# Performance work log

Measured on AMD Instinct MI355X. Metric: run time of the kernel, lower is better.

Reference implementation:

```python
import jax, jax.numpy as jnp
import numpy as np

# ---- module configuration (from init_kwargs) ----
NX, NV = 2048, 1024
LX = 1.0
VMAX = 6.0
DX = LX / NX
DV = 2.0 * VMAX / NV
XS = jnp.linspace(-LX / 2 + DX / 2, LX / 2 - DX / 2, NX)
VS = jnp.linspace(-VMAX + DV / 2, VMAX - DV / 2, NV)
AE, AI = 1.0, 1836.0
ZE, ZI = -1.0, 1.0
OMEGA_C_TAU = 1.0
NU_EE, NU_II = 1.0, 0.1
DT = 1e-3
T_LBO = 1.0  # LBO temperature, u = 0


def minmod(a, b):
    return jnp.where(a * b > 0, jnp.sign(a) * jnp.minimum(jnp.abs(a), jnp.abs(b)), 0.0)


def _sl(a, lo, hi, axis):
    return jax.lax.slice_in_dim(a, lo, hi, axis=axis)


def slope_limited_flux_divergence(f_pad, F, dx, axis):
    # f_pad has N+4 cells along `axis` (2 ghost cells per side). MUSCL + minmod.
    n = f_pad.shape[axis]
    d = _sl(f_pad, 1, n, axis) - _sl(f_pad, 0, n - 1, axis)          # n-1 diffs
    sigma = minmod(_sl(d, 0, n - 2, axis), _sl(d, 1, n - 1, axis))    # slopes for cells 1..n-2
    fc = _sl(f_pad, 1, n - 1, axis)                                   # cells 1..n-2
    m = n - 2
    fL = _sl(fc, 0, m - 1, axis) + 0.5 * _sl(sigma, 0, m - 1, axis)   # left interface states
    fR = _sl(fc, 1, m, axis) - 0.5 * _sl(sigma, 1, m, axis)           # right interface states
    flux = F(fL, fR)                                                  # N+1 interface fluxes
    k = flux.shape[axis]
    return (_sl(flux, 1, k, axis) - _sl(flux, 0, k - 1, axis)) / dx   # N cells


def pad_x_periodic(f):
    return jnp.concatenate([f[-2:, :], f, f[:2, :]], axis=0)


def pad_v_zero(f):
    z = jnp.zeros((f.shape[0], 2), f.dtype)
    return jnp.concatenate([z, f, z], axis=1)


def poisson_solve(rho_c):
    # dE/dx = rho_c, zero-mean E (periodic-compatible gauge)
    E = jnp.cumsum(rho_c) * DX
    return E - jnp.mean(E)


def species_rhs(f, E, A, Z):
    v = VS[None, :]
    Fx = lambda l, r: jnp.where(v > 0, l * v, r * v)                  # upwind in x
    vdfdx = slope_limited_flux_divergence(pad_x_periodic(f), Fx, DX, axis=0)
    Ec = (OMEGA_C_TAU * Z / A) * E[:, None]
    Fv = lambda l, r: jnp.where(Ec > 0, l * Ec, r * Ec)               # upwind in v
    Edfdv = slope_limited_flux_divergence(pad_v_zero(f), Fv, DV, axis=1)
    return -vdfdx - Edfdv


def vlasov_rhs(fe, fi):
    ne = jnp.sum(fe, axis=1) * DV
    ni = jnp.sum(fi, axis=1) * DV
    E = poisson_solve(ZE * ne + ZI * ni)
    return species_rhs(fe, E, AE, ZE), species_rhs(fi, E, AI, ZI)


def ssprk2(fe, fi, dt):
    re, ri = vlasov_rhs(fe, fi)
    fe1, fi1 = fe + dt * re, fi + dt * ri
    re1, ri1 = vlasov_rhs(fe1, fi1)
    return 0.5 * (fe + fe1 + dt * re1), 0.5 * (fi + fi1 + dt * ri1)


def lbo_diagonals(lam):
    # L f = lam * d/dv( v f + T df/dv ), central differences
    vm = jnp.roll(VS, 1)
    vp = jnp.roll(VS, -1)
    dl = lam * (T_LBO / DV**2 - vm / (2 * DV))
    du = lam * (T_LBO / DV**2 + vp / (2 * DV))
    d = lam * (-2.0 * T_LBO / DV**2) * jnp.ones(NV, XS.dtype)
    return dl.at[0].set(0.0), d, du.at[-1].set(0.0)


def nu_shape():
    midpt = LX / 3
    ef = LX / 6 / 10
    h0 = lambda x: 1 + jnp.exp(x / ef - midpt / ef)
    return 1.0 / (0.5 * (h0(XS) + h0(-XS)))  # [Nx]


def thomas(dl, d, du, b):
    # Thomas algorithm; dl[0]==0 and du[-1]==0 assumed.
    def fwd(carry, inp):
        cp, bp = carry
        dli, di, dui, bi = inp
        m = di - dli * cp
        cpi = dui / m
        bpi = (bi - dli * bp) / m
        return (cpi, bpi), (cpi, bpi)
    z = jnp.zeros((), b.dtype)
    _, (cp, bp) = jax.lax.scan(fwd, (z, z), (dl, d, du, b))
    def bwd(x_next, inp):
        cpi, bpi = inp
        x = bpi - cpi * x_next
        return x, x
    _, x = jax.lax.scan(bwd, z, (cp, bp), reverse=True)
    return x


def implicit_collide(f, lam, dt):
    dl, d, du = lbo_diagonals(lam)
    nu = nu_shape()
    def solve_row(nui, frow):
        return thomas(-dt * nui * dl, 1.0 - dt * nui * d, -dt * nui * du, frow)
    return jax.vmap(solve_row)(nu, f)


def setup_inputs() -> dict:
    key = jax.random.key(0)
    k1, k2 = jax.random.split(key)
    fe = jax.random.uniform(k1, (NX, NV), dtype=jnp.float32)
    fi = jax.random.uniform(k2, (NX, NV), dtype=jnp.float32)
    return {"fe": fe, "fi": fi}


def reference(fe, fi):
    fe1, fi1 = ssprk2(fe, fi, DT)
    fe2 = implicit_collide(fe1, NU_EE, DT)
    fi2 = implicit_collide(fi1, NU_II, DT)
    return jnp.stack([fe2, fi2])  # [2, Nx, Nv]
```

## Files before the change

kernel.cpp:

```cpp
#include <hip/hip_runtime.h>
#include <math.h>

#define NX 2048
#define NV 1024

static constexpr float DXf    = 1.0f / 2048.0f;
static constexpr float DVf    = 12.0f / 1024.0f;
static constexpr float DTf    = 0.001f;
static constexpr float INV_DX = 2048.0f;
static constexpr float INV_DV = 1024.0f / 12.0f;

__device__ __forceinline__ float minmod_f(float a, float b) {
    return (a * b > 0.0f) ? (a > 0.0f ? fminf(a, b) : fmaxf(a, b)) : 0.0f;
}

__device__ __forceinline__ float frcp(float x) {
    float r = __builtin_amdgcn_rcpf(x);
    return r * (2.0f - x * r);
}

__device__ __forceinline__ int swz512(int x) {
    return ((x & 7) << 6) + (x >> 3);
}

__device__ __forceinline__ void rhs4(const float* __restrict__ g, int i, int j0, float Ec,
                                     float4& f0v, float4& rv) {
    const float* rowc = g + i * NV;
    const float* rm1  = g + (((i - 1) & (NX - 1)) * NV);
    const float* rm2  = g + (((i - 2) & (NX - 1)) * NV);
    const float* rp1  = g + (((i + 1) & (NX - 1)) * NV);
    const float* rp2  = g + (((i + 2) & (NX - 1)) * NV);

    float4 c   = *(const float4*)(rowc + j0);
    float4 xm1 = *(const float4*)(rm1 + j0);
    float4 xm2 = *(const float4*)(rm2 + j0);
    float4 xp1 = *(const float4*)(rp1 + j0);
    float4 xp2 = *(const float4*)(rp2 + j0);
    float4 lm = make_float4(0.f, 0.f, 0.f, 0.f);
    float4 rp = make_float4(0.f, 0.f, 0.f, 0.f);
    if (j0 >= 4)      lm = *(const float4*)(rowc + j0 - 4);
    if (j0 <= NV - 8) rp = *(const float4*)(rowc + j0 + 4);

    float vals[8] = {lm.z, lm.w, c.x, c.y, c.z, c.w, rp.x, rp.y};
    const float* cc   = (const float*)&c;
    const float* am1  = (const float*)&xm1;
    const float* am2  = (const float*)&xm2;
    const float* ap1  = (const float*)&xp1;
    const float* ap2  = (const float*)&xp2;
    float* f0o = (float*)&f0v;
    float* ro  = (float*)&rv;

    #pragma unroll
    for (int k = 0; k < 4; ++k) {
        float f0  = cc[k];
        float fm1 = am1[k], fm2 = am2[k], fp1 = ap1[k], fp2 = ap2[k];

        float v = DVf * ((float)(j0 + k) + 0.5f) - 6.0f;
        float dm1 = fm1 - fm2, d0 = f0 - fm1, dp1 = fp1 - f0, dp2 = fp2 - fp1;
        float sm1 = minmod_f(dm1, d0);
        float s0  = minmod_f(d0, dp1);
        float sp1 = minmod_f(dp1, dp2);
        float PhiM, PhiP;
        if (v > 0.0f) {
            PhiM = (fm1 + 0.5f * sm1) * v;
            PhiP = (f0  + 0.5f * s0 ) * v;
        } else {
            PhiM = (f0  - 0.5f * s0 ) * v;
            PhiP = (fp1 - 0.5f * sp1) * v;
        }
        float vdfdx = (PhiP - PhiM) * INV_DX;

        float gm2 = vals[k], gm1 = vals[k + 1], gp1 = vals[k + 3], gp2 = vals[k + 4];
        float em1 = gm1 - gm2, e0 = f0 - gm1, ep1 = gp1 - f0, ep2 = gp2 - gp1;
        float tm1 = minmod_f(em1, e0);
        float t0  = minmod_f(e0, ep1);
        float tp1 = minmod_f(ep1, ep2);
        float GM, GP;
        if (Ec > 0.0f) {
            GM = (gm1 + 0.5f * tm1) * Ec;
            GP = (f0  + 0.5f * t0 ) * Ec;
        } else {
            GM = (f0  - 0.5f * t0 ) * Ec;
            GP = (gp1 - 0.5f * tp1) * Ec;
        }
        float Edfdv = (GP - GM) * INV_DV;

        f0o[k] = f0;
        ro[k]  = -vdfdx - Edfdv;
    }
}

__device__ __forceinline__ float block_E(const float* __restrict__ se_,
                                         const float* __restrict__ si_,
                                         int r0, int wv) {
    int t = threadIdx.x;
    int i3 = r0 + 3;
    float pref = 0.0f, wtot = 0.0f;
    #pragma unroll
    for (int q = 0; q < NX / 256; ++q) {
        int k = q * 256 + t;
        float rho = DVf * (si_[k] - se_[k]);
        if (k <= i3) pref += rho;
        wtot += rho * (float)(NX - k);
    }
    #pragma unroll
    for (int off = 32; off > 0; off >>= 1) {
        pref += __shfl_down(pref, off, 64);
        wtot += __shfl_down(wtot, off, 64);
    }
    __shared__ float sp_[4], sw_[4];
    int lane = t & 63, wave = t >> 6;
    if (lane == 0) { sp_[wave] = pref; sw_[wave] = wtot; }
    __syncthreads();
    float P3 = sp_[0] + sp_[1] + sp_[2] + sp_[3];
    float W  = sw_[0] + sw_[1] + sw_[2] + sw_[3];
    float rho1 = DVf * (si_[r0 + 1] - se_[r0 + 1]);
    float rho2 = DVf * (si_[r0 + 2] - se_[r0 + 2]);
    float rho3 = DVf * (si_[r0 + 3] - se_[r0 + 3]);
    float corr = (wv == 3) ? 0.0f
               : (wv == 2) ? rho3
               : (wv == 1) ? (rho3 + rho2)
                           : (rho3 + rho2 + rho1);
    return DXf * (P3 - corr - W * (1.0f / (float)NX));
}

__global__ __launch_bounds__(256) void moments_kernel(const float* __restrict__ fe,
                                                      const float* __restrict__ fi,
                                                      float* __restrict__ se,
                                                      float* __restrict__ si) {
    const int g = swz512(blockIdx.x);
    const int t = threadIdx.x, lane = t & 63, wv = t >> 6;
    const int row = (g << 2) + wv;
    const float* rpe = fe + row * NV;
    const float* rpi = fi + row * NV;
    float a = 0.0f, b = 0.0f;
    #pragma unroll
    for (int q = 0; q < 4; ++q) {
        float4 x = *(const float4*)(rpe + 4 * lane + 256 * q);
        float4 y = *(const float4*)(rpi + 4 * lane + 256 * q);
        a += x.x + x.y + x.z + x.w;
        b += y.x + y.y + y.z + y.w;
    }
    #pragma unroll
    for (int off = 32; off > 0; off >>= 1) {
        a += __shfl_down(a, off, 64);
        b += __shfl_down(b, off, 64);
    }
    if (lane == 0) { se[row] = a; si[row] = b; }
}

__global__ __launch_bounds__(256) void stage1_kernel(const float* __restrict__ fe,
                                                     const float* __restrict__ fi,
                                                     const float* __restrict__ se,
                                                     const float* __restrict__ si,
                                                     float* __restrict__ fe1,
                                                     float* __restrict__ fi1,
                                                     float* __restrict__ se1,
                                                     float* __restrict__ si1) {
    const int g  = swz512(blockIdx.x);
    const int sp = blockIdx.y;
    const int r0 = g << 2;
    const int t = threadIdx.x, lane = t & 63, wv = t >> 6;
    const float* f = sp ? fi : fe;
    float* f1 = sp ? fi1 : fe1;
    const float zoa = sp ? (1.0f / 1836.0f) : -1.0f;
    const float Ec = zoa * block_E(se, si, r0, wv);
    const int row = r0 + wv;

    float s = 0.0f;
    #pragma unroll
    for (int q = 0; q < 4; ++q) {
        const int j0 = 4 * lane + 256 * q;
        float4 f0v, rv;
        rhs4(f, row, j0, Ec, f0v, rv);
        float4 o;
        o.x = f0v.x + DTf * rv.x;
        o.y = f0v.y + DTf * rv.y;
        o.z = f0v.z + DTf * rv.z;
        o.w = f0v.w + DTf * rv.w;
        *(float4*)(f1 + row * NV + j0) = o;
        s += o.x + o.y + o.z + o.w;
    }
    #pragma unroll
    for (int off = 32; off > 0; off >>= 1) s += __shfl_down(s, off, 64);
    if (lane == 0) (sp ? si1 : se1)[row] = s;
}

__global__ __launch_bounds__(256) void stage2_collide_kernel(
    const float* __restrict__ fe, const float* __restrict__ fi,
    const float* __restrict__ fe1, const float* __restrict__ fi1,
    const float* __restrict__ se1, const float* __restrict__ si1,
    float* __restrict__ out) {
    const int g  = swz512(blockIdx.x);
    const int sp = blockIdx.y;
    const int r0 = g << 2;
    const int t = threadIdx.x, lane = t & 63, wv = t >> 6;
    const float* h  = sp ? fi : fe;
    const float* f1 = sp ? fi1 : fe1;
    const float zoa = sp ? (1.0f / 1836.0f) : -1.0f;
    const float lam = sp ? 0.1f : 1.0f;
    const float Ec = zoa * block_E(se1, si1, r0, wv);
    const int row = r0 + wv;
    float* orow = out + ((size_t)sp * NX + row) * NV;

    const float Tdv2   = 1.0f / (DVf * DVf);
    const float inv2dv = 0.5f / DVf;
    const float xi = DXf * ((float)row + 0.5f) - 0.5f;
    const float nu = 1.0f / (1.0f + 0.5f * (expf(60.0f * xi - 20.0f) + expf(-60.0f * xi - 20.0f)));
    const float K = DTf * nu * lam;
    const float b = 1.0f + 2.0f * K * Tdv2;

    const int j0 = 16 * lane;

    float Dv[16], Av[16], Cv[16];
    #pragma unroll
    for (int q = 0; q < 4; ++q) {
        float4 f0v, rv;
        rhs4(f1, row, j0 + 4 * q, Ec, f0v, rv);
        float4 h4 = *(const float4*)(h + row * NV + j0 + 4 * q);
        float dq[4];
        dq[0] = 0.5f * h4.x + 0.5f * f0v.x + (0.5f * DTf) * rv.x;
        dq[1] = 0.5f * h4.y + 0.5f * f0v.y + (0.5f * DTf) * rv.y;
        dq[2] = 0.5f * h4.z + 0.5f * f0v.z + (0.5f * DTf) * rv.z;
        dq[3] = 0.5f * h4.w + 0.5f * f0v.w + (0.5f * DTf) * rv.w;
        #pragma unroll
        for (int rr = 0; rr < 4; ++rr) {
            const int r = 4 * q + rr;
            const int j = j0 + r;
            float a = (j == 0)      ? 0.0f : -K * (Tdv2 - (DVf * ((float)j - 0.5f) - 6.0f) * inv2dv);
            float c = (j == NV - 1) ? 0.0f : -K * (Tdv2 + (DVf * ((float)j + 1.5f) - 6.0f) * inv2dv);
            if (r == 0) {
                float e = frcp(b);
                Dv[0] = e * dq[0];
                Av[0] = e * a;
                Cv[0] = e * c;
            } else {
                float e = frcp(b - a * Cv[r - 1]);
                Dv[r] = e * (dq[rr] - a * Dv[r - 1]);
                Av[r] = -e * a * Av[r - 1];
                Cv[r] = e * c;
            }
        }
    }
    #pragma unroll
    for (int r = 14; r >= 0; --r) {
        Dv[r] = Dv[r] - Cv[r] * Dv[r + 1];
        Av[r] = Av[r] - Cv[r] * Av[r + 1];
        Cv[r] = -Cv[r] * Cv[r + 1];
    }

    float la = Av[0],  ra = Cv[0],  d0 = Dv[0];
    float lb = Av[15], rb = Cv[15], d1 = Dv[15];
    #pragma unroll
    for (int s = 1; s < 64; s <<= 1) {
        float lb_m = __shfl_up(lb, s, 64);
        float rb_m = __shfl_up(rb, s, 64);
        float d1_m = __shfl_up(d1, s, 64);
        if (lane < s) { lb_m = 0.0f; rb_m = 0.0f; d1_m = 0.0f; }
        float la_p = __shfl_down(la, s, 64);
        float ra_p = __shfl_down(ra, s, 64);
        float d0_p = __shfl_down(d0, s, 64);
        if (lane + s > 63) { la_p = 0.0f; ra_p = 0.0f; d0_p = 0.0f; }

        float m00 = 1.0f - la * rb_m;
        float m01 = -ra * la_p;
        float m10 = -lb * rb_m;
        float m11 = 1.0f - rb * la_p;
        float idet = frcp(m00 * m11 - m01 * m10);

        float Lr0 = -la * lb_m, Lr1 = -lb * lb_m;
        float Rr0 = -ra * ra_p, Rr1 = -rb * ra_p;
        float e0 = d0 - la * d1_m - ra * d0_p;
        float e1 = d1 - lb * d1_m - rb * d0_p;

        la = idet * (m11 * Lr0 - m01 * Lr1);
        lb = idet * (m00 * Lr1 - m10 * Lr0);
        ra = idet * (m11 * Rr0 - m01 * Rr1);
        rb = idet * (m00 * Rr1 - m10 * Rr0);
        d0 = idet * (m11 * e0 - m01 * e1);
        d1 = idet * (m00 * e1 - m10 * e0);
    }
    float zl = __shfl_up(d1, 1, 64);
    if (lane == 0) zl = 0.0f;
    float yr = __shfl_down(d0, 1, 64);
    if (lane == 63) yr = 0.0f;

    #pragma unroll
    for (int r = 0; r < 16; ++r) Dv[r] = Dv[r] - Av[r] * zl - Cv[r] * yr;
    #pragma unroll
    for (int q = 0; q < 4; ++q) {
        float4 o;
        o.x = Dv[4 * q + 0];
        o.y = Dv[4 * q + 1];
        o.z = Dv[4 * q + 2];
        o.w = Dv[4 * q + 3];
        *(float4*)(orow + j0 + 4 * q) = o;
    }
}

extern "C" void kernel_launch(void* const* d_in, const int* in_sizes, int n_in,
                              void* d_out, int out_size, void* d_ws, size_t ws_size,
                              hipStream_t stream) {
    const float* fe = (const float*)d_in[0];
    const float* fi = (const float*)d_in[1];
    float* out = (float*)d_out;
    const size_t P = (size_t)NX * NV;

    float* fe1 = (float*)d_ws;
    float* fi1 = fe1 + P;
    float* se  = fi1 + P;
    float* si  = se + NX;
    float* se1 = si + NX;
    float* si1 = se1 + NX;

    dim3 rgrid(512, 2);

    moments_kernel<<<512, 256, 0, stream>>>(fe, fi, se, si);
    stage1_kernel<<<rgrid, 256, 0, stream>>>(fe, fi, se, si, fe1, fi1, se1, si1);
    stage2_collide_kernel<<<rgrid, 256, 0, stream>>>(fe, fi, fe1, fi1, se1, si1, out);
}
```

Measured before the change: 127.5 us.

## Precompute E field via single-block scan kernel and use one row per block

Replaces the per-block redundant reduction over all 2048 charge densities (block_E) with a separate single-block prefix-scan kernel that writes E once per stage. The stage kernels then read E[row] directly, and the grid is restructured so each block handles one row (256 threads for moments/stage1, one 64-thread wave for stage2), giving 4x more blocks. This removes redundant per-block work and a barrier, at the cost of two extra serial tiny launches and smaller blocks.

```diff
diff --git a/kernel.cpp b/kernel.cpp
--- a/kernel.cpp
+++ b/kernel.cpp
@@ -19,8 +19,8 @@
     return r * (2.0f - x * r);
 }
 
-__device__ __forceinline__ int swz512(int x) {
-    return ((x & 7) << 6) + (x >> 3);
+__device__ __forceinline__ int swz2048(int x) {
+    return ((x & 7) << 8) + (x >> 3);
 }
 
 __device__ __forceinline__ void rhs4(const float* __restrict__ g, int i, int j0, float Ec,
@@ -90,117 +90,122 @@
     }
 }
 
-__device__ __forceinline__ float block_E(const float* __restrict__ se_,
-                                         const float* __restrict__ si_,
-                                         int r0, int wv) {
-    int t = threadIdx.x;
-    int i3 = r0 + 3;
-    float pref = 0.0f, wtot = 0.0f;
-    #pragma unroll
-    for (int q = 0; q < NX / 256; ++q) {
-        int k = q * 256 + t;
-        float rho = DVf * (si_[k] - se_[k]);
-        if (k <= i3) pref += rho;
-        wtot += rho * (float)(NX - k);
-    }
-    #pragma unroll
-    for (int off = 32; off > 0; off >>= 1) {
-        pref += __shfl_down(pref, off, 64);
-        wtot += __shfl_down(wtot, off, 64);
-    }
-    __shared__ float sp_[4], sw_[4];
-    int lane = t & 63, wave = t >> 6;
-    if (lane == 0) { sp_[wave] = pref; sw_[wave] = wtot; }
-    __syncthreads();
-    float P3 = sp_[0] + sp_[1] + sp_[2] + sp_[3];
-    float W  = sw_[0] + sw_[1] + sw_[2] + sw_[3];
-    float rho1 = DVf * (si_[r0 + 1] - se_[r0 + 1]);
-    float rho2 = DVf * (si_[r0 + 2] - se_[r0 + 2]);
-    float rho3 = DVf * (si_[r0 + 3] - se_[r0 + 3]);
-    float corr = (wv == 3) ? 0.0f
-               : (wv == 2) ? rho3
-               : (wv == 1) ? (rho3 + rho2)
-                           : (rho3 + rho2 + rho1);
-    return DXf * (P3 - corr - W * (1.0f / (float)NX));
-}
-
 __global__ __launch_bounds__(256) void moments_kernel(const float* __restrict__ fe,
                                                       const float* __restrict__ fi,
                                                       float* __restrict__ se,
                                                       float* __restrict__ si) {
-    const int g = swz512(blockIdx.x);
+    const int row = swz2048(blockIdx.x);
     const int t = threadIdx.x, lane = t & 63, wv = t >> 6;
-    const int row = (g << 2) + wv;
-    const float* rpe = fe + row * NV;
-    const float* rpi = fi + row * NV;
-    float a = 0.0f, b = 0.0f;
-    #pragma unroll
-    for (int q = 0; q < 4; ++q) {
-        float4 x = *(const float4*)(rpe + 4 * lane + 256 * q);
-        float4 y = *(const float4*)(rpi + 4 * lane + 256 * q);
-        a += x.x + x.y + x.z + x.w;
-        b += y.x + y.y + y.z + y.w;
-    }
+    float4 x = *(const float4*)(fe + (size_t)row * NV + 4 * t);
+    float4 y = *(const float4*)(fi + (size_t)row * NV + 4 * t);
+    float a = x.x + x.y + x.z + x.w;
+    float b = y.x + y.y + y.z + y.w;
     #pragma unroll
     for (int off = 32; off > 0; off >>= 1) {
         a += __shfl_down(a, off, 64);
         b += __shfl_down(b, off, 64);
     }
-    if (lane == 0) { se[row] = a; si[row] = b; }
+    __shared__ float r1[4], r2[4];
+    if (lane == 0) { r1[wv] = a; r2[wv] = b; }
+    __syncthreads();
+    if (t == 0) {
+        se[row] = r1[0] + r1[1] + r1[2] + r1[3];
+        si[row] = r2[0] + r2[1] + r2[2] + r2[3];
+    }
+}
+
+__global__ __launch_bounds__(256) void escan_kernel(const float* __restrict__ se_,
+                                                    const float* __restrict__ si_,
+                                                    float* __restrict__ E) {
+    const int t = threadIdx.x, lane = t & 63, wv = t >> 6;
+    const int k0 = t * 8;
+    float4 a0 = *(const float4*)(se_ + k0);
+    float4 a1 = *(const float4*)(se_ + k0 + 4);
+    float4 b0 = *(const float4*)(si_ + k0);
+    float4 b1 = *(const float4*)(si_ + k0 + 4);
+    float rho[8];
+    rho[0] = DVf * (b0.x - a0.x); rho[1] = DVf * (b0.y - a0.y);
+    rho[2] = DVf * (b0.z - a0.z); rho[3] = DVf * (b0.w - a0.w);
+    rho[4] = DVf * (b1.x - a1.x); rho[5] = DVf * (b1.y - a1.y);
+    rho[6] = DVf * (b1.z - a1.z); rho[7] = DVf * (b1.w - a1.w);
+    float s = 0.0f, w = 0.0f;
+    #pragma unroll
+    for (int r = 0; r < 8; ++r) {
+        s += rho[r];
+        w += rho[r] * (float)(NX - (k0 + r));
+    }
+    float sc = s;
+    #pragma unroll
+    for (int off = 1; off < 64; off <<= 1) {
+        float u = __shfl_up(sc, off, 64);
+        if (lane >= off) sc += u;
+    }
+    #pragma unroll
+    for (int off = 32; off > 0; off >>= 1) w += __shfl_down(w, off, 64);
+    __shared__ float wsum[4], wtot[4];
+    if (lane == 63) wsum[wv] = sc;
+    if (lane == 0)  wtot[wv] = w;
+    __syncthreads();
+    float base = 0.0f;
+    #pragma unroll
+    for (int u = 0; u < 4; ++u) if (u < wv) base += wsum[u];
+    float W = wtot[0] + wtot[1] + wtot[2] + wtot[3];
+    float run = base + sc - s;
+    const float mean = W * (1.0f / (float)NX);
+    #pragma unroll
+    for (int r = 0; r < 8; ++r) {
+        run += rho[r];
+        E[k0 + r] = DXf * (run - mean);
+    }
 }
 
 __global__ __launch_bounds__(256) void stage1_kernel(const float* __restrict__ fe,
                                                      const float* __restrict__ fi,
-                                                     const float* __restrict__ se,
-                                                     const float* __restrict__ si,
+                                                     const float* __restrict__ E0,
                                                      float* __restrict__ fe1,
                                                      float* __restrict__ fi1,
                                                      float* __restrict__ se1,
                                                      float* __restrict__ si1) {
-    const int g  = swz512(blockIdx.x);
-    const int sp = blockIdx.y;
-    const int r0 = g << 2;
-    const int t = threadIdx.x, lane = t & 63, wv = t >> 6;
+    const int row = swz2048(blockIdx.x);
+    const int sp  = blockIdx.y;
     const float* f = sp ? fi : fe;
     float* f1 = sp ? fi1 : fe1;
     const float zoa = sp ? (1.0f / 1836.0f) : -1.0f;
-    const float Ec = zoa * block_E(se, si, r0, wv);
-    const int row = r0 + wv;
-
-    float s = 0.0f;
-    #pragma unroll
-    for (int q = 0; q < 4; ++q) {
-        const int j0 = 4 * lane + 256 * q;
-        float4 f0v, rv;
-        rhs4(f, row, j0, Ec, f0v, rv);
-        float4 o;
-        o.x = f0v.x + DTf * rv.x;
-        o.y = f0v.y + DTf * rv.y;
-        o.z = f0v.z + DTf * rv.z;
-        o.w = f0v.w + DTf * rv.w;
-        *(float4*)(f1 + row * NV + j0) = o;
-        s += o.x + o.y + o.z + o.w;
-    }
+    const float Ec = zoa * E0[row];
+    const int t = threadIdx.x, lane = t & 63, wv = t >> 6;
+    const int j0 = 4 * t;
+
+    float4 f0v, rv;
+    rhs4(f, row, j0, Ec, f0v, rv);
+    float4 o;
+    o.x = f0v.x + DTf * rv.x;
+    o.y = f0v.y + DTf * rv.y;
+    o.z = f0v.z + DTf * rv.z;
+    o.w = f0v.w + DTf * rv.w;
+    *(float4*)(f1 + (size_t)row * NV + j0) = o;
+
+    float s = o.x + o.y + o.z + o.w;
     #pragma unroll
     for (int off = 32; off > 0; off >>= 1) s += __shfl_down(s, off, 64);
-    if (lane == 0) (sp ? si1 : se1)[row] = s;
-}
-
-__global__ __launch_bounds__(256) void stage2_collide_kernel(
+    __shared__ float sred[4];
+    if (lane == 0) sred[wv] = s;
+    __syncthreads();
+    if (t == 0) (sp ? si1 : se1)[row] = sred[0] + sred[1] + sred[2] + sred[3];
+}
+
+__global__ __launch_bounds__(64) void stage2_collide_kernel(
     const float* __restrict__ fe, const float* __restrict__ fi,
     const float* __restrict__ fe1, const float* __restrict__ fi1,
-    const float* __restrict__ se1, const float* __restrict__ si1,
+    const float* __restrict__ E1,
     float* __restrict__ out) {
-    const int g  = swz512(blockIdx.x);
-    const int sp = blockIdx.y;
-    const int r0 = g << 2;
-    const int t = threadIdx.x, lane = t & 63, wv = t >> 6;
+    const int row = swz2048(blockIdx.x);
+    const int sp  = blockIdx.y;
+    const int lane = threadIdx.x & 63;
     const float* h  = sp ? fi : fe;
     const float* f1 = sp ? fi1 : fe1;
     const float zoa = sp ? (1.0f / 1836.0f) : -1.0f;
     const float lam = sp ? 0.1f : 1.0f;
-    const float Ec = zoa * block_E(se1, si1, r0, wv);
-    const int row = r0 + wv;
+    const float Ec = zoa * E1[row];
     float* orow = out + ((size_t)sp * NX + row) * NV;
 
     const float Tdv2   = 1.0f / (DVf * DVf);
@@ -217,7 +222,7 @@
     for (int q = 0; q < 4; ++q) {
         float4 f0v, rv;
         rhs4(f1, row, j0 + 4 * q, Ec, f0v, rv);
-        float4 h4 = *(const float4*)(h + row * NV + j0 + 4 * q);
+        float4 h4 = *(const float4*)(h + (size_t)row * NV + j0 + 4 * q);
         float dq[4];
         dq[0] = 0.5f * h4.x + 0.5f * f0v.x + (0.5f * DTf) * rv.x;
         dq[1] = 0.5f * h4.y + 0.5f * f0v.y + (0.5f * DTf) * rv.y;
@@ -312,10 +317,14 @@
     float* si  = se + NX;
     float* se1 = si + NX;
     float* si1 = se1 + NX;
-
-    dim3 rgrid(512, 2);
-
-    moments_kernel<<<512, 256, 0, stream>>>(fe, fi, se, si);
-    stage1_kernel<<<rgrid, 256, 0, stream>>>(fe, fi, se, si, fe1, fi1, se1, si1);
-    stage2_collide_kernel<<<rgrid, 256, 0, stream>>>(fe, fi, fe1, fi1, se1, si1, out);
-}
+    float* E0  = si1 + NX;
+    float* E1  = E0 + NX;
+
+    dim3 rgrid(2048, 2);
+
+    moments_kernel<<<2048, 256, 0, stream>>>(fe, fi, se, si);
+    escan_kernel<<<1, 256, 0, stream>>>(se, si, E0);
+    stage1_kernel<<<rgrid, 256, 0, stream>>>(fe, fi, E0, fe1, fi1, se1, si1);
+    escan_kernel<<<1, 256, 0, stream>>>(se1, si1, E1);
+    stage2_collide_kernel<<<rgrid, 64, 0, stream>>>(fe, fi, fe1, fi1, E1, out);
+}
```

After: 115.3 us. 9.6% less time.
